# Kernel tuning notes

Measured on AMD Instinct MI355X. Metric: run time of the kernel, lower is better.

The kernel has to match this reference:

```python
import jax, jax.numpy as jnp
import numpy as np

NUM_CLASSES = 50000
FEAT_DIM = 256
BATCH = 131072
LAMBDA_CENT = 0.5
EPS = 1e-12  # matches F.normalize default eps


def setup_inputs() -> dict:
    key = jax.random.key(0)
    k1, k2, k3 = jax.random.split(key, 3)
    features = jax.random.normal(k1, (BATCH, FEAT_DIM), dtype=jnp.float32)
    labels = jax.random.randint(k2, (BATCH,), 0, NUM_CLASSES)
    centers = jax.random.normal(k3, (NUM_CLASSES, FEAT_DIM), dtype=jnp.float32)
    return {"features": features, "labels": labels, "centers": centers}


def reference(features, labels, centers):
    # L2 normalize rows (F.normalize, p=2, dim=1)
    norms = jnp.linalg.norm(features, axis=1, keepdims=True)
    f = features / jnp.maximum(norms, EPS)
    # gather centers per sample: [B, D]
    cb = centers[labels]
    loss_cent = jnp.sum((f - cb) ** 2) / features.shape[0]
    # training-mode center update, vectorized:
    # torch loop: delta[labels[i]] += (cb[i] - f[i]) / (1 + count(labels == labels[i]))
    cnt = jax.ops.segment_sum(jnp.ones(labels.shape, f.dtype), labels,
                              num_segments=NUM_CLASSES)  # [C]
    w = 1.0 / (1.0 + cnt[labels])  # [B]
    delta = jax.ops.segment_sum((cb - f) * w[:, None], labels,
                                num_segments=NUM_CLASSES)  # [C, D]
    new_centers = centers - LAMBDA_CENT * delta
    return loss_cent, new_centers
```

## Files before the change

### kernel.cpp

```cpp
#include <hip/hip_runtime.h>
#include <hip/hip_bf16.h>
#include <math.h>

#define BATCH   131072
#define FEAT    256
#define NCLASS  50000
#define EPS     1e-12f
#define LAMBDA  0.5f
#define CAP     32

constexpr int WPB     = 4;
constexpr int NBLK_NS = BATCH  / WPB;
constexpr int NBLK_SS = NCLASS / WPB;
constexpr int NSCAN   = (NCLASS + 255) / 256;


__device__ __forceinline__ float wave_reduce_sum(float v) {
    #pragma unroll
    for (int m = 32; m; m >>= 1) v += __shfl_xor(v, m, 64);
    return v;
}

__global__ __launch_bounds__(256) void histo(const int* __restrict__ labels,
                                             int* __restrict__ cnt) {
    const int i = blockIdx.x * 256 + threadIdx.x;
    atomicAdd(&cnt[labels[i]], 1);
}

__global__ __launch_bounds__(256) void scan_bsum(const int* __restrict__ cnt,
                                                 int* __restrict__ bsum) {
    __shared__ int s[256];
    const int i = blockIdx.x * 256 + threadIdx.x;
    s[threadIdx.x] = (i < NCLASS) ? cnt[i] : 0;
    __syncthreads();
    for (int off = 128; off; off >>= 1) {
        if (threadIdx.x < off) s[threadIdx.x] += s[threadIdx.x + off];
        __syncthreads();
    }
    if (threadIdx.x == 0) bsum[blockIdx.x] = s[0];
}

__global__ __launch_bounds__(256) void scan_boff(const int* __restrict__ bsum,
                                                 int* __restrict__ boff) {
    __shared__ int s[256];
    const int t = threadIdx.x;
    const int v = (t < NSCAN) ? bsum[t] : 0;
    s[t] = v;
    __syncthreads();
    for (int off = 1; off < 256; off <<= 1) {
        int u = (t >= off) ? s[t - off] : 0;
        __syncthreads();
        s[t] += u;
        __syncthreads();
    }
    if (t < NSCAN) boff[t] = s[t] - v;
}

__global__ __launch_bounds__(256) void scan_final(const int* __restrict__ cnt,
                                                  const int* __restrict__ boff,
                                                  int* __restrict__ cursor) {
    __shared__ int s[256];
    const int t = threadIdx.x;
    const int i = blockIdx.x * 256 + t;
    const int v = (i < NCLASS) ? cnt[i] : 0;
    s[t] = v;
    __syncthreads();
    for (int off = 1; off < 256; off <<= 1) {
        int u = (t >= off) ? s[t - off] : 0;
        __syncthreads();
        s[t] += u;
        __syncthreads();
    }
    if (i < NCLASS) cursor[i] = s[t] - v + boff[blockIdx.x];
}

__global__ __launch_bounds__(256) void norm_scatter(
        const float* __restrict__ feat,
        const int*   __restrict__ labels,
        int*         __restrict__ cursor,
        int*         __restrict__ sIdx,
        float*       __restrict__ rinvS,
        float*       __restrict__ pA) {
    const int wave = threadIdx.x >> 6;
    const int lane = threadIdx.x & 63;
    const int row  = blockIdx.x * WPB + wave;

    const float4 v = ((const float4*)(feat + (size_t)row * FEAT))[lane];
    const float ss = wave_reduce_sum(v.x*v.x + v.y*v.y + v.z*v.z + v.w*v.w);
    const float rinv = 1.0f / fmaxf(sqrtf(ss), EPS);

    if (lane == 0) {
        const int slot = atomicAdd(&cursor[labels[row]], 1);
        sIdx[slot]  = row;
        rinvS[slot] = rinv;
    }

    __shared__ float red[WPB];
    if (lane == 0) red[wave] = ss * rinv * rinv;
    __syncthreads();
    if (threadIdx.x == 0)
        pA[blockIdx.x] = red[0] + red[1] + red[2] + red[3];
}

__global__ __launch_bounds__(256) void segsum_gather2(
        const float* __restrict__ feat,
        const float* __restrict__ centers,
        const int*   __restrict__ cnt,
        const int*   __restrict__ cursor_end,
        const int*   __restrict__ sIdx,
        const float* __restrict__ rinvS,
        float*       __restrict__ outc,
        float*       __restrict__ pB) {
    const int wave = threadIdx.x >> 6;
    const int lane = threadIdx.x & 63;
    const int c    = blockIdx.x * WPB + wave;

    const int n     = cnt[c];
    const int start = cursor_end[c] - n;

    float4 acc = {0.f, 0.f, 0.f, 0.f};

    for (int base = 0; base < n; base += 64) {
        const int cn = min(64, n - base);
        int   myidx = 0;
        float myrv  = 0.f;
        if (lane < cn) {
            myidx = sIdx [start + base + lane];
            myrv  = rinvS[start + base + lane];
        }

        for (int s = 0; s < cn; s += 8) {
            #pragma unroll
            for (int k = 0; k < 8; ++k) {
                const int   r  = __shfl(myidx, s + k, 64);
                const float rv = __shfl(myrv,  s + k, 64);
                const float4 v = ((const float4*)(feat + (size_t)r * FEAT))[lane];
                acc.x += v.x * rv;
                acc.y += v.y * rv;
                acc.z += v.z * rv;
                acc.w += v.w * rv;
            }
        }
    }

    const float4 cv = ((const float4*)(centers + (size_t)c * FEAT))[lane];
    const float fn = (float)n;
    const float w  = 1.0f / (1.0f + fn);

    float4 nc;
    nc.x = cv.x - LAMBDA * (fn * cv.x - acc.x) * w;
    nc.y = cv.y - LAMBDA * (fn * cv.y - acc.y) * w;
    nc.z = cv.z - LAMBDA * (fn * cv.z - acc.z) * w;
    nc.w = cv.w - LAMBDA * (fn * cv.w - acc.w) * w;
    ((float4*)(outc + (size_t)c * FEAT))[lane] = nc;

    float lp = fn * (cv.x*cv.x + cv.y*cv.y + cv.z*cv.z + cv.w*cv.w)
             - 2.0f * (acc.x*cv.x + acc.y*cv.y + acc.z*cv.z + acc.w*cv.w);
    lp = wave_reduce_sum(lp);

    __shared__ float red[WPB];
    if (lane == 0) red[wave] = lp;
    __syncthreads();
    if (threadIdx.x == 0)
        pB[blockIdx.x] = red[0] + red[1] + red[2] + red[3];
}

__global__ __launch_bounds__(1024) void finish(const float* __restrict__ pA,
                                               const float* __restrict__ pB,
                                               float* __restrict__ out0) {
    float s = 0.0f;
    for (int i = threadIdx.x; i < NBLK_NS; i += 1024) s += pA[i];
    for (int i = threadIdx.x; i < NBLK_SS; i += 1024) s += pB[i];
    s = wave_reduce_sum(s);
    __shared__ float red[16];
    const int wave = threadIdx.x >> 6;
    const int lane = threadIdx.x & 63;
    if (lane == 0) red[wave] = s;
    __syncthreads();
    if (threadIdx.x == 0) {
        float t = 0.0f;
        #pragma unroll
        for (int i = 0; i < 16; ++i) t += red[i];
        out0[0] = t * (1.0f / (float)BATCH);
    }
}


__global__ __launch_bounds__(256) void scatter_bucket(const int* __restrict__ labels,
                                                      int* __restrict__ cnt,
                                                      int* __restrict__ bucket) {
    const int i = blockIdx.x * 256 + threadIdx.x;
    const int c = labels[i];
    const int slot = atomicAdd(&cnt[c], 1);
    if (slot < CAP) bucket[c * CAP + slot] = i;
}

__global__ __launch_bounds__(256) void gather_bucket(
        const float* __restrict__ feat, const float* __restrict__ centers,
        const int* __restrict__ cnt, const int* __restrict__ bucket,
        float* __restrict__ outc, float* __restrict__ pB) {
    const int wave = threadIdx.x >> 6;
    const int lane = threadIdx.x & 63;
    const int c    = blockIdx.x * WPB + wave;
    const int n = min(cnt[c], CAP);
    const int myidx = (lane < n) ? bucket[c * CAP + lane] : 0;
    float4 acc = {0.f,0.f,0.f,0.f};
    float fsum2 = 0.f;
    for (int s = 0; s < n; ++s) {
        const int r = __shfl(myidx, s, 64);
        const float4 v = ((const float4*)(feat + (size_t)r * FEAT))[lane];
        float ss = wave_reduce_sum(v.x*v.x + v.y*v.y + v.z*v.z + v.w*v.w);
        const float rinv = 1.0f / fmaxf(sqrtf(ss), EPS);
        acc.x += v.x*rinv; acc.y += v.y*rinv; acc.z += v.z*rinv; acc.w += v.w*rinv;
        fsum2 += ss * rinv * rinv;
    }
    const float4 cv = ((const float4*)(centers + (size_t)c * FEAT))[lane];
    const float fn = (float)n;
    const float w  = 1.0f / (1.0f + fn);
    float4 nc;
    nc.x = cv.x - LAMBDA * (fn*cv.x - acc.x) * w;
    nc.y = cv.y - LAMBDA * (fn*cv.y - acc.y) * w;
    nc.z = cv.z - LAMBDA * (fn*cv.z - acc.z) * w;
    nc.w = cv.w - LAMBDA * (fn*cv.w - acc.w) * w;
    ((float4*)(outc + (size_t)c * FEAT))[lane] = nc;
    float lp = fn * (cv.x*cv.x + cv.y*cv.y + cv.z*cv.z + cv.w*cv.w)
             - 2.0f * (acc.x*cv.x + acc.y*cv.y + acc.z*cv.z + acc.w*cv.w);
    lp = wave_reduce_sum(lp);
    __shared__ float red[WPB];
    if (lane == 0) red[wave] = lp + fsum2;
    __syncthreads();
    if (threadIdx.x == 0)
        pB[blockIdx.x] = red[0] + red[1] + red[2] + red[3];
}

__global__ __launch_bounds__(1024) void finishB(const float* __restrict__ pB,
                                                float* __restrict__ out0) {
    float s = 0.0f;
    for (int i = threadIdx.x; i < NBLK_SS; i += 1024) s += pB[i];
    s = wave_reduce_sum(s);
    __shared__ float red[16];
    const int wave = threadIdx.x >> 6;
    const int lane = threadIdx.x & 63;
    if (lane == 0) red[wave] = s;
    __syncthreads();
    if (threadIdx.x == 0) {
        float t = 0.0f;
        #pragma unroll
        for (int i = 0; i < 16; ++i) t += red[i];
        out0[0] = t * (1.0f / (float)BATCH);
    }
}

extern "C" void kernel_launch(void* const* d_in, const int* in_sizes, int n_in,
                              void* d_out, int out_size, void* d_ws, size_t ws_size,
                              hipStream_t stream) {
    const float* feat    = (const float*)d_in[0];
    const int*   labels  = (const int*)  d_in[1];
    const float* centers = (const float*)d_in[2];
    float* out = (float*)d_out;

    const size_t need_fast =
        ((size_t)NCLASS * 2 + 512 + NBLK_NS + NBLK_SS + (size_t)BATCH * 2) * 4;

    if (ws_size >= need_fast) {
        int*   cnt    = (int*)d_ws;
        int*   cursor = cnt + NCLASS;
        int*   bsum   = cursor + NCLASS;
        int*   boff   = bsum + 256;
        float* pA     = (float*)(boff + 256);
        float* pB     = pA + NBLK_NS;
        int*   sIdx   = (int*)(pB + NBLK_SS);
        float* rinvS  = (float*)(sIdx + BATCH);

        hipMemsetAsync(cnt, 0, NCLASS * sizeof(int), stream);
        histo      <<<BATCH / 256, 256, 0, stream>>>(labels, cnt);
        scan_bsum  <<<NSCAN, 256, 0, stream>>>(cnt, bsum);
        scan_boff  <<<1, 256, 0, stream>>>(bsum, boff);
        scan_final <<<NSCAN, 256, 0, stream>>>(cnt, boff, cursor);
        norm_scatter<<<NBLK_NS, 256, 0, stream>>>(feat, labels, cursor,
                                                  sIdx, rinvS, pA);
        segsum_gather2<<<NBLK_SS, 256, 0, stream>>>(feat, centers, cnt, cursor,
                                                    sIdx, rinvS, out + 1, pB);
        finish<<<1, 1024, 0, stream>>>(pA, pB, out);
    } else {
        int*   cnt    = (int*)d_ws;
        int*   bucket = cnt + NCLASS;
        float* pB     = (float*)(bucket + (size_t)NCLASS * CAP);
        hipMemsetAsync(cnt, 0, NCLASS * sizeof(int), stream);
        scatter_bucket<<<BATCH / 256, 256, 0, stream>>>(labels, cnt, bucket);
        gather_bucket <<<NBLK_SS, 256, 0, stream>>>(feat, centers, cnt, bucket,
                                                    out + 1, pB);
        finishB<<<1, 1024, 0, stream>>>(pB, out);
    }
}
```

Measured before the change: 294.8 us.

## Replace sort-and-gather segment sum with direct float atomic scatter into outputs

Drops the prefix-scan, index-scatter and segmented-gather passes. Each center row is first scaled by (1 - λ·n/(1+n)) and written to the output. Each feature row is then normalized and its weighted contribution is added into its center's output row with per-element float atomics. The loss is split algebraically into per-sample terms (‖f‖² - 2 f·c) and per-class n‖c‖² terms. This removes several launches and the second random read of features. In exchange it adds 131072×256 global float atomics and makes the summation order nondeterministic.

```diff
diff --git a/kernel.cpp b/kernel.cpp
--- a/kernel.cpp
+++ b/kernel.cpp
@@ -1,5 +1,4 @@
 #include <hip/hip_runtime.h>
-#include <hip/hip_bf16.h>
 #include <math.h>
 
 #define BATCH   131072
@@ -7,12 +6,10 @@
 #define NCLASS  50000
 #define EPS     1e-12f
 #define LAMBDA  0.5f
-#define CAP     32
 
-constexpr int WPB     = 4;
-constexpr int NBLK_NS = BATCH  / WPB;
-constexpr int NBLK_SS = NCLASS / WPB;
-constexpr int NSCAN   = (NCLASS + 255) / 256;
+constexpr int WPB    = 4;
+constexpr int NBLK_M = BATCH  / WPB;
+constexpr int NBLK_C = NCLASS / WPB;
 
 
 __device__ __forceinline__ float wave_reduce_sum(float v) {
@@ -27,216 +24,81 @@
     atomicAdd(&cnt[labels[i]], 1);
 }
 
-__global__ __launch_bounds__(256) void scan_bsum(const int* __restrict__ cnt,
-                                                 int* __restrict__ bsum) {
-    __shared__ int s[256];
-    const int i = blockIdx.x * 256 + threadIdx.x;
-    s[threadIdx.x] = (i < NCLASS) ? cnt[i] : 0;
-    __syncthreads();
-    for (int off = 128; off; off >>= 1) {
-        if (threadIdx.x < off) s[threadIdx.x] += s[threadIdx.x + off];
-        __syncthreads();
-    }
-    if (threadIdx.x == 0) bsum[blockIdx.x] = s[0];
-}
-
-__global__ __launch_bounds__(256) void scan_boff(const int* __restrict__ bsum,
-                                                 int* __restrict__ boff) {
-    __shared__ int s[256];
-    const int t = threadIdx.x;
-    const int v = (t < NSCAN) ? bsum[t] : 0;
-    s[t] = v;
-    __syncthreads();
-    for (int off = 1; off < 256; off <<= 1) {
-        int u = (t >= off) ? s[t - off] : 0;
-        __syncthreads();
-        s[t] += u;
-        __syncthreads();
-    }
-    if (t < NSCAN) boff[t] = s[t] - v;
-}
-
-__global__ __launch_bounds__(256) void scan_final(const int* __restrict__ cnt,
-                                                  const int* __restrict__ boff,
-                                                  int* __restrict__ cursor) {
-    __shared__ int s[256];
-    const int t = threadIdx.x;
-    const int i = blockIdx.x * 256 + t;
-    const int v = (i < NCLASS) ? cnt[i] : 0;
-    s[t] = v;
-    __syncthreads();
-    for (int off = 1; off < 256; off <<= 1) {
-        int u = (t >= off) ? s[t - off] : 0;
-        __syncthreads();
-        s[t] += u;
-        __syncthreads();
-    }
-    if (i < NCLASS) cursor[i] = s[t] - v + boff[blockIdx.x];
-}
-
-__global__ __launch_bounds__(256) void norm_scatter(
-        const float* __restrict__ feat,
-        const int*   __restrict__ labels,
-        int*         __restrict__ cursor,
-        int*         __restrict__ sIdx,
-        float*       __restrict__ rinvS,
-        float*       __restrict__ pA) {
-    const int wave = threadIdx.x >> 6;
-    const int lane = threadIdx.x & 63;
-    const int row  = blockIdx.x * WPB + wave;
-
-    const float4 v = ((const float4*)(feat + (size_t)row * FEAT))[lane];
-    const float ss = wave_reduce_sum(v.x*v.x + v.y*v.y + v.z*v.z + v.w*v.w);
-    const float rinv = 1.0f / fmaxf(sqrtf(ss), EPS);
-
-    if (lane == 0) {
-        const int slot = atomicAdd(&cursor[labels[row]], 1);
-        sIdx[slot]  = row;
-        rinvS[slot] = rinv;
-    }
-
-    __shared__ float red[WPB];
-    if (lane == 0) red[wave] = ss * rinv * rinv;
-    __syncthreads();
-    if (threadIdx.x == 0)
-        pA[blockIdx.x] = red[0] + red[1] + red[2] + red[3];
-}
-
-__global__ __launch_bounds__(256) void segsum_gather2(
-        const float* __restrict__ feat,
+__global__ __launch_bounds__(256) void scale_out(
         const float* __restrict__ centers,
         const int*   __restrict__ cnt,
-        const int*   __restrict__ cursor_end,
-        const int*   __restrict__ sIdx,
-        const float* __restrict__ rinvS,
         float*       __restrict__ outc,
-        float*       __restrict__ pB) {
+        float*       __restrict__ pC) {
     const int wave = threadIdx.x >> 6;
     const int lane = threadIdx.x & 63;
     const int c    = blockIdx.x * WPB + wave;
 
-    const int n     = cnt[c];
-    const int start = cursor_end[c] - n;
-
-    float4 acc = {0.f, 0.f, 0.f, 0.f};
-
-    for (int base = 0; base < n; base += 64) {
-        const int cn = min(64, n - base);
-        int   myidx = 0;
-        float myrv  = 0.f;
-        if (lane < cn) {
-            myidx = sIdx [start + base + lane];
-            myrv  = rinvS[start + base + lane];
-        }
-
-        for (int s = 0; s < cn; s += 8) {
-            #pragma unroll
-            for (int k = 0; k < 8; ++k) {
-                const int   r  = __shfl(myidx, s + k, 64);
-                const float rv = __shfl(myrv,  s + k, 64);
-                const float4 v = ((const float4*)(feat + (size_t)r * FEAT))[lane];
-                acc.x += v.x * rv;
-                acc.y += v.y * rv;
-                acc.z += v.z * rv;
-                acc.w += v.w * rv;
-            }
-        }
-    }
-
     const float4 cv = ((const float4*)(centers + (size_t)c * FEAT))[lane];
-    const float fn = (float)n;
-    const float w  = 1.0f / (1.0f + fn);
+    const float fn = (float)cnt[c];
+    const float s1 = 1.0f - LAMBDA * fn / (1.0f + fn);
 
     float4 nc;
-    nc.x = cv.x - LAMBDA * (fn * cv.x - acc.x) * w;
-    nc.y = cv.y - LAMBDA * (fn * cv.y - acc.y) * w;
-    nc.z = cv.z - LAMBDA * (fn * cv.z - acc.z) * w;
-    nc.w = cv.w - LAMBDA * (fn * cv.w - acc.w) * w;
+    nc.x = cv.x * s1; nc.y = cv.y * s1; nc.z = cv.z * s1; nc.w = cv.w * s1;
     ((float4*)(outc + (size_t)c * FEAT))[lane] = nc;
 
-    float lp = fn * (cv.x*cv.x + cv.y*cv.y + cv.z*cv.z + cv.w*cv.w)
-             - 2.0f * (acc.x*cv.x + acc.y*cv.y + acc.z*cv.z + acc.w*cv.w);
+    float lp = fn * (cv.x*cv.x + cv.y*cv.y + cv.z*cv.z + cv.w*cv.w);
     lp = wave_reduce_sum(lp);
 
     __shared__ float red[WPB];
     if (lane == 0) red[wave] = lp;
     __syncthreads();
     if (threadIdx.x == 0)
-        pB[blockIdx.x] = red[0] + red[1] + red[2] + red[3];
+        pC[blockIdx.x] = red[0] + red[1] + red[2] + red[3];
+}
+
+__global__ __launch_bounds__(256) void norm_atomic(
+        const float* __restrict__ feat,
+        const int*   __restrict__ labels,
+        const float* __restrict__ centers,
+        const int*   __restrict__ cnt,
+        float*       __restrict__ outc,
+        float*       __restrict__ pA) {
+    const int wave = threadIdx.x >> 6;
+    const int lane = threadIdx.x & 63;
+    const int row  = blockIdx.x * WPB + wave;
+
+    const float4 v   = ((const float4*)(feat + (size_t)row * FEAT))[lane];
+    const int    lbl = labels[row];
+    const float4 cv  = ((const float4*)(centers + (size_t)lbl * FEAT))[lane];
+
+    float a = v.x*v.x + v.y*v.y + v.z*v.z + v.w*v.w;
+    float b = v.x*cv.x + v.y*cv.y + v.z*cv.z + v.w*cv.w;
+    #pragma unroll
+    for (int m = 32; m; m >>= 1) {
+        a += __shfl_xor(a, m, 64);
+        b += __shfl_xor(b, m, 64);
+    }
+
+    const float rinv = 1.0f / fmaxf(sqrtf(a), EPS);
+    const float w    = 1.0f / (1.0f + (float)cnt[lbl]);
+    const float coef = LAMBDA * w * rinv;
+
+    float* dst = outc + (size_t)lbl * FEAT + lane * 4;
+    atomicAdd(dst + 0, v.x * coef);
+    atomicAdd(dst + 1, v.y * coef);
+    atomicAdd(dst + 2, v.z * coef);
+    atomicAdd(dst + 3, v.w * coef);
+
+    const float lp = (a * rinv) * rinv - 2.0f * (b * rinv);
+
+    __shared__ float red[WPB];
+    if (lane == 0) red[wave] = lp;
+    __syncthreads();
+    if (threadIdx.x == 0)
+        pA[blockIdx.x] = red[0] + red[1] + red[2] + red[3];
 }
 
 __global__ __launch_bounds__(1024) void finish(const float* __restrict__ pA,
-                                               const float* __restrict__ pB,
+                                               const float* __restrict__ pC,
                                                float* __restrict__ out0) {
     float s = 0.0f;
-    for (int i = threadIdx.x; i < NBLK_NS; i += 1024) s += pA[i];
-    for (int i = threadIdx.x; i < NBLK_SS; i += 1024) s += pB[i];
-    s = wave_reduce_sum(s);
-    __shared__ float red[16];
-    const int wave = threadIdx.x >> 6;
-    const int lane = threadIdx.x & 63;
-    if (lane == 0) red[wave] = s;
-    __syncthreads();
-    if (threadIdx.x == 0) {
-        float t = 0.0f;
-        #pragma unroll
-        for (int i = 0; i < 16; ++i) t += red[i];
-        out0[0] = t * (1.0f / (float)BATCH);
-    }
-}
-
-
-__global__ __launch_bounds__(256) void scatter_bucket(const int* __restrict__ labels,
-                                                      int* __restrict__ cnt,
-                                                      int* __restrict__ bucket) {
-    const int i = blockIdx.x * 256 + threadIdx.x;
-    const int c = labels[i];
-    const int slot = atomicAdd(&cnt[c], 1);
-    if (slot < CAP) bucket[c * CAP + slot] = i;
-}
-
-__global__ __launch_bounds__(256) void gather_bucket(
-        const float* __restrict__ feat, const float* __restrict__ centers,
-        const int* __restrict__ cnt, const int* __restrict__ bucket,
-        float* __restrict__ outc, float* __restrict__ pB) {
-    const int wave = threadIdx.x >> 6;
-    const int lane = threadIdx.x & 63;
-    const int c    = blockIdx.x * WPB + wave;
-    const int n = min(cnt[c], CAP);
-    const int myidx = (lane < n) ? bucket[c * CAP + lane] : 0;
-    float4 acc = {0.f,0.f,0.f,0.f};
-    float fsum2 = 0.f;
-    for (int s = 0; s < n; ++s) {
-        const int r = __shfl(myidx, s, 64);
-        const float4 v = ((const float4*)(feat + (size_t)r * FEAT))[lane];
-        float ss = wave_reduce_sum(v.x*v.x + v.y*v.y + v.z*v.z + v.w*v.w);
-        const float rinv = 1.0f / fmaxf(sqrtf(ss), EPS);
-        acc.x += v.x*rinv; acc.y += v.y*rinv; acc.z += v.z*rinv; acc.w += v.w*rinv;
-        fsum2 += ss * rinv * rinv;
-    }
-    const float4 cv = ((const float4*)(centers + (size_t)c * FEAT))[lane];
-    const float fn = (float)n;
-    const float w  = 1.0f / (1.0f + fn);
-    float4 nc;
-    nc.x = cv.x - LAMBDA * (fn*cv.x - acc.x) * w;
-    nc.y = cv.y - LAMBDA * (fn*cv.y - acc.y) * w;
-    nc.z = cv.z - LAMBDA * (fn*cv.z - acc.z) * w;
-    nc.w = cv.w - LAMBDA * (fn*cv.w - acc.w) * w;
-    ((float4*)(outc + (size_t)c * FEAT))[lane] = nc;
-    float lp = fn * (cv.x*cv.x + cv.y*cv.y + cv.z*cv.z + cv.w*cv.w)
-             - 2.0f * (acc.x*cv.x + acc.y*cv.y + acc.z*cv.z + acc.w*cv.w);
-    lp = wave_reduce_sum(lp);
-    __shared__ float red[WPB];
-    if (lane == 0) red[wave] = lp + fsum2;
-    __syncthreads();
-    if (threadIdx.x == 0)
-        pB[blockIdx.x] = red[0] + red[1] + red[2] + red[3];
-}
-
-__global__ __launch_bounds__(1024) void finishB(const float* __restrict__ pB,
-                                                float* __restrict__ out0) {
-    float s = 0.0f;
-    for (int i = threadIdx.x; i < NBLK_SS; i += 1024) s += pB[i];
+    for (int i = threadIdx.x; i < NBLK_M; i += 1024) s += pA[i];
+    for (int i = threadIdx.x; i < NBLK_C; i += 1024) s += pC[i];
     s = wave_reduce_sum(s);
     __shared__ float red[16];
     const int wave = threadIdx.x >> 6;
@@ -259,37 +121,14 @@
     const float* centers = (const float*)d_in[2];
     float* out = (float*)d_out;
 
-    const size_t need_fast =
-        ((size_t)NCLASS * 2 + 512 + NBLK_NS + NBLK_SS + (size_t)BATCH * 2) * 4;
+    int*   cnt = (int*)d_ws;
+    float* pA  = (float*)(cnt + NCLASS);
+    float* pC  = pA + NBLK_M;
 
-    if (ws_size >= need_fast) {
-        int*   cnt    = (int*)d_ws;
-        int*   cursor = cnt + NCLASS;
-        int*   bsum   = cursor + NCLASS;
-        int*   boff   = bsum + 256;
-        float* pA     = (float*)(boff + 256);
-        float* pB     = pA + NBLK_NS;
-        int*   sIdx   = (int*)(pB + NBLK_SS);
-        float* rinvS  = (float*)(sIdx + BATCH);
-
-        hipMemsetAsync(cnt, 0, NCLASS * sizeof(int), stream);
-        histo      <<<BATCH / 256, 256, 0, stream>>>(labels, cnt);
-        scan_bsum  <<<NSCAN, 256, 0, stream>>>(cnt, bsum);
-        scan_boff  <<<1, 256, 0, stream>>>(bsum, boff);
-        scan_final <<<NSCAN, 256, 0, stream>>>(cnt, boff, cursor);
-        norm_scatter<<<NBLK_NS, 256, 0, stream>>>(feat, labels, cursor,
-                                                  sIdx, rinvS, pA);
-        segsum_gather2<<<NBLK_SS, 256, 0, stream>>>(feat, centers, cnt, cursor,
-                                                    sIdx, rinvS, out + 1, pB);
-        finish<<<1, 1024, 0, stream>>>(pA, pB, out);
-    } else {
-        int*   cnt    = (int*)d_ws;
-        int*   bucket = cnt + NCLASS;
-        float* pB     = (float*)(bucket + (size_t)NCLASS * CAP);
-        hipMemsetAsync(cnt, 0, NCLASS * sizeof(int), stream);
-        scatter_bucket<<<BATCH / 256, 256, 0, stream>>>(labels, cnt, bucket);
-        gather_bucket <<<NBLK_SS, 256, 0, stream>>>(feat, centers, cnt, bucket,
-                                                    out + 1, pB);
-        finishB<<<1, 1024, 0, stream>>>(pB, out);
-    }
+    hipMemsetAsync(cnt, 0, NCLASS * sizeof(int), stream);
+    histo      <<<BATCH / 256, 256, 0, stream>>>(labels, cnt);
+    scale_out  <<<NBLK_C, 256, 0, stream>>>(centers, cnt, out + 1, pC);
+    norm_atomic<<<NBLK_M, 256, 0, stream>>>(feat, labels, centers, cnt,
+                                            out + 1, pA);
+    finish<<<1, 1024, 0, stream>>>(pA, pC, out);
 }
```

Measured after the change: 659.6 us. 124% more time.
